# Kernel optimization log

Hardware: AMD Instinct MI355X
Metric: run time of the kernel (lower is better)

## Reference

```python
import jax, jax.numpy as jnp
import numpy as np

B, N, K, S_IN, S_OUT, C, FD = 32, 325, 20, 12, 12, 10, 64
ALPHA = 0.5  # LeakyReLU negative slope

def leaky(x):
    return jnp.where(x >= 0, x, ALPHA * x)

def setup_inputs() -> dict:
    key = jax.random.key(0)
    ks = jax.random.split(key, 9)
    s = 0.2
    return {
        "fushed_features": jax.random.normal(ks[0], (B, N, FD), jnp.float32),
        "input_data": jax.random.normal(ks[1], (B, N, S_IN), jnp.float32),
        "w_W": jax.random.normal(ks[2], (S_IN, S_OUT), jnp.float32) * s,
        "w_b": jax.random.normal(ks[3], (S_OUT,), jnp.float32) * s,
        "a1_W": jax.random.normal(ks[4], (2 * S_OUT, 4 * S_OUT), jnp.float32) * s,
        "a1_b": jax.random.normal(ks[5], (4 * S_OUT,), jnp.float32) * s,
        "a2_W": jax.random.normal(ks[6], (4 * S_OUT, C), jnp.float32) * s,
        "a2_b": jax.random.normal(ks[7], (C,), jnp.float32) * s,
        "adj_mx_topk_index": jax.random.randint(ks[8], (B, N, K), 0, N),
    }

def reference(fushed_features, input_data, w_W, w_b, a1_W, a1_b, a2_W, a2_b, adj_mx_topk_index):
    # w_net: Linear + LeakyReLU -> wh [B,N,S_OUT]
    wh = leaky(input_data @ w_W + w_b)
    # a_net on cat([wh_i, wh_j]): split first linear to avoid materializing [B,N,N,2*S_OUT]
    hx = wh @ a1_W[:S_OUT]   # contribution of wh_x (row node i)
    hy = wh @ a1_W[S_OUT:]   # contribution of wh_y (col node j)
    hidden = leaky(hx[:, :, None, :] + hy[:, None, :, :] + a1_b)   # [B,N,N,4*S_OUT]
    attention = leaky(hidden @ a2_W + a2_b)                        # [B,N,N,C]
    idx = adj_mx_topk_index                                        # [B,N,K]
    # gather top-k neighbors along dim 2
    idx_c = jnp.broadcast_to(idx[..., None], idx.shape + (attention.shape[-1],))
    attention_mask = jnp.take_along_axis(attention, idx_c, axis=2)  # [B,N,K,C]
    attention_mask = jax.nn.softmax(attention_mask, axis=-1)
    # gather neighbor features: wh_expand_top_k[b,i,k] = wh[b, idx[b,i,k]]
    wh_topk = wh[jnp.arange(wh.shape[0])[:, None, None], idx]       # [B,N,K,S_OUT]
    # output = attention_mask^T @ wh_topk
    output_data = jnp.einsum('bnkc,bnks->bncs', attention_mask, wh_topk)
    # clustering loss on detached neighbor features (cosine similarity)
    wt = jax.lax.stop_gradient(wh_topk)
    wtn = wt / (jnp.linalg.norm(wt, axis=-1, keepdims=True) + 1e-8)
    dist_mat = jnp.einsum('bnks,bnls->bnkl', wtn, wtn)              # [B,N,K,K]
    same = (dist_mat >= 0.5).astype(dist_mat.dtype)
    diff = 1.0 - same
    prob = jnp.einsum('bnkc,bnlc->bnkl', attention_mask, attention_mask)
    prob = jnp.clip(prob, 1e-4, 1.0 - 1e-4)
    logp = jnp.log(prob)
    cl = -(same * logp - diff * logp)
    cluster_loss = (cl.sum((-1, -2)) - jnp.trace(cl, axis1=-2, axis2=-1)).mean()
    return output_data, cluster_loss, dist_mat.mean(), wh.mean()
```

## Files before the change

### kernel.cpp

```cpp
#include <hip/hip_runtime.h>
#include <math.h>

#define Bdim 32
#define Ndim 325
#define Kdim 20
#define Sdim 12
#define Cdim 10
#define Hdim 48
#define NB   (Bdim*Ndim)
#define OUT_SCALARS (NB*Cdim*Sdim)
#define Tpairs (Kdim*(Kdim-1)/2)
#define BN_BLOCKS (NB/4)
#define NODE_BLOCKS 260
#define NPB 40

#define O_WH  0
#define O_HX  (O_WH + NB*Sdim)
#define O_HY  (O_HX + NB*Hdim)
#define O_PCL (O_HY + NB*Hdim)
#define O_PDS (O_PCL + BN_BLOCKS)
#define O_PWH (O_PDS + BN_BLOCKS)
#define WS_BASE_FLOATS (O_PWH + NODE_BLOCKS)

__device__ __forceinline__ float leaky(float x) { return x >= 0.f ? x : 0.5f * x; }

__global__ __launch_bounds__(512)
void node_kernel(const float* __restrict__ x,
                 const float* __restrict__ wW, const float* __restrict__ wb,
                 const float* __restrict__ A1, const float* __restrict__ b1,
                 float* __restrict__ ws)
{
    __shared__ float s_wh[NPB][Sdim];
    __shared__ float s_r[8];
    const int tid = threadIdx.x;
    const int base = blockIdx.x * NPB;

    float v = 0.f;
    if (tid < NPB * Sdim) {
        const int n = tid / Sdim, s = tid - n * Sdim;
        const float* xr = x + (size_t)(base + n) * Sdim;
        float acc = wb[s];
        #pragma unroll
        for (int i = 0; i < Sdim; i++) acc += xr[i] * wW[i * Sdim + s];
        acc = leaky(acc);
        s_wh[n][s] = acc;
        ws[O_WH + (size_t)(base + n) * Sdim + s] = acc;
        v += acc;
    }
    __syncthreads();

    #pragma unroll
    for (int rep = 0; rep < 8; rep++) {
        const int e = tid + rep * 512;
        if (e < NPB * 96) {
            const int n = e / 96, r = e - n * 96;
            const int which = r / Hdim, d = r - which * Hdim;
            const float4 w0 = *(const float4*)&s_wh[n][0];
            const float4 w1 = *(const float4*)&s_wh[n][4];
            const float4 w2 = *(const float4*)&s_wh[n][8];
            const float* Ac = A1 + (which * Sdim) * Hdim + d;
            float acc = which ? 0.f : b1[d];
            acc += w0.x*Ac[0*Hdim] + w0.y*Ac[1*Hdim] + w0.z*Ac[2*Hdim] + w0.w*Ac[3*Hdim]
                 + w1.x*Ac[4*Hdim] + w1.y*Ac[5*Hdim] + w1.z*Ac[6*Hdim] + w1.w*Ac[7*Hdim]
                 + w2.x*Ac[8*Hdim] + w2.y*Ac[9*Hdim] + w2.z*Ac[10*Hdim] + w2.w*Ac[11*Hdim];
            ws[(which ? O_HY : O_HX) + (size_t)(base + n) * Hdim + d] = acc;
        }
    }

    #pragma unroll
    for (int off = 32; off > 0; off >>= 1) v += __shfl_down(v, off);
    if ((tid & 63) == 0) s_r[tid >> 6] = v;
    __syncthreads();
    if (tid == 0) {
        float t = 0.f;
        #pragma unroll
        for (int i = 0; i < 8; i++) t += s_r[i];
        ws[O_PWH + blockIdx.x] = t;
    }
}

__global__ __launch_bounds__(256)
void mega_kernel(const int* __restrict__ topk,
                 const float* __restrict__ A2, const float* __restrict__ b2,
                 float* __restrict__ ws, float* __restrict__ out)
{
    __shared__ float s_A2  [Hdim * 12];
    __shared__ float s_whj [4][Kdim][12];
    __shared__ float s_am  [4][Kdim][12];
    __shared__ float s_invn[4][Kdim];
    __shared__ float s_red[2][4];

    const int tid = threadIdx.x;
    const int slot = tid >> 6, t = tid & 63;

    #pragma unroll
    for (int e = tid; e < Hdim * Cdim; e += 256) {
        const int d = e / Cdim, c = e - d * Cdim;
        s_A2[d * 12 + c] = A2[e];
    }
    __syncthreads();

    if (tid < 160) {
        const int e = tid >> 1, half = tid & 1;
        const int gid = blockIdx.x * 80 + e;
        const int bn_e = gid / Kdim;
        const int b_e  = bn_e / Ndim;
        const int j    = topk[gid];
        const int ek   = e / 20, kk = e - ek * 20;

        const float4* hx4 = (const float4*)(ws + O_HX + (size_t)bn_e * Hdim) + half * 6;
        const float4* hy4 = (const float4*)(ws + O_HY + ((size_t)b_e * Ndim + j) * Hdim) + half * 6;

        float acc[Cdim];
        #pragma unroll
        for (int c = 0; c < Cdim; c++) acc[c] = 0.f;
        #pragma unroll
        for (int q = 0; q < 6; q++) {
            const float4 xv = hx4[q], yv = hy4[q];
            const float hh[4] = { leaky(xv.x + yv.x), leaky(xv.y + yv.y),
                                  leaky(xv.z + yv.z), leaky(xv.w + yv.w) };
            #pragma unroll
            for (int i = 0; i < 4; i++) {
                const int d = half * 24 + q * 4 + i;
                const float* Ar = &s_A2[d * 12];
                const float4 r0 = *(const float4*)(Ar + 0);
                const float4 r1 = *(const float4*)(Ar + 4);
                const float2 r2 = *(const float2*)(Ar + 8);
                const float h = hh[i];
                acc[0] += h * r0.x; acc[1] += h * r0.y;
                acc[2] += h * r0.z; acc[3] += h * r0.w;
                acc[4] += h * r1.x; acc[5] += h * r1.y;
                acc[6] += h * r1.z; acc[7] += h * r1.w;
                acc[8] += h * r2.x; acc[9] += h * r2.y;
            }
        }
        float full[Cdim];
        #pragma unroll
        for (int c = 0; c < Cdim; c++) full[c] = acc[c] + __shfl_xor(acc[c], 1);
        if (half == 0) {
            float m = -1e30f;
            #pragma unroll
            for (int c = 0; c < Cdim; c++) { full[c] = leaky(full[c] + b2[c]); m = fmaxf(m, full[c]); }
            float sum = 0.f;
            #pragma unroll
            for (int c = 0; c < Cdim; c++) { full[c] = __expf(full[c] - m); sum += full[c]; }
            const float inv = 1.f / sum;
            *(float4*)&s_am[ek][kk][0] = make_float4(full[0]*inv, full[1]*inv, full[2]*inv, full[3]*inv);
            *(float4*)&s_am[ek][kk][4] = make_float4(full[4]*inv, full[5]*inv, full[6]*inv, full[7]*inv);
            *(float4*)&s_am[ek][kk][8] = make_float4(full[8]*inv, full[9]*inv, 0.f, 0.f);
        }
    } else {
        for (int i = tid - 160; i < 240; i += 96) {
            const int kf = i / 3, q = i - kf * 3;
            const int sl = kf / 20, k = kf - sl * 20;
            const int gidx = blockIdx.x * 80 + kf;
            const int bn_i = gidx / Kdim;
            const int b_i  = bn_i / Ndim;
            const int j    = topk[gidx];
            const float4 v = *(const float4*)(ws + O_WH + ((size_t)b_i * Ndim + j) * Sdim + q * 4);
            *(float4*)&s_whj[sl][k][q * 4] = v;
        }
    }
    __syncthreads();

    const int bn = blockIdx.x * 4 + slot;
    float cl = 0.f, ds = 0.f;

    if (t < Kdim) {
        const float4 w0 = *(const float4*)&s_whj[slot][t][0];
        const float4 w1 = *(const float4*)&s_whj[slot][t][4];
        const float4 w2 = *(const float4*)&s_whj[slot][t][8];
        const float nn = w0.x*w0.x + w0.y*w0.y + w0.z*w0.z + w0.w*w0.w
                       + w1.x*w1.x + w1.y*w1.y + w1.z*w1.z + w1.w*w1.w
                       + w2.x*w2.x + w2.y*w2.y + w2.z*w2.z + w2.w*w2.w;
        const float invn = 1.f / (sqrtf(nn) + 1e-8f);
        s_invn[slot][t] = invn;
        ds += nn * invn * invn;
    } else if (t < Kdim + 30) {
        const int e = t - Kdim, c = e / 3, sq = e - c * 3;
        float4 o = make_float4(0.f, 0.f, 0.f, 0.f);
        #pragma unroll
        for (int k = 0; k < Kdim; k++) {
            const float a = s_am[slot][k][c];
            const float4 w = *(const float4*)&s_whj[slot][k][sq * 4];
            o.x += a * w.x; o.y += a * w.y; o.z += a * w.z; o.w += a * w.w;
        }
        *(float4*)(out + (size_t)bn * (Cdim * Sdim) + c * Sdim + sq * 4) = o;
    }
    __builtin_amdgcn_wave_barrier();

    #pragma unroll
    for (int it = 0; it < 3; it++) {
        const int e = t + it * 64;
        if (e < Tpairs) {
            const int r = Tpairs - 1 - e;
            const int m = (int)((sqrtf((float)(8 * r + 1)) - 1.f) * 0.5f + 1e-4f);
            const int k = Kdim - 2 - m;
            const int l = Kdim - 1 - (r - (m * (m + 1)) / 2);

            const float4 a0 = *(const float4*)&s_whj[slot][k][0];
            const float4 a1 = *(const float4*)&s_whj[slot][k][4];
            const float4 a2 = *(const float4*)&s_whj[slot][k][8];
            const float4 c0 = *(const float4*)&s_whj[slot][l][0];
            const float4 c1 = *(const float4*)&s_whj[slot][l][4];
            const float4 c2 = *(const float4*)&s_whj[slot][l][8];
            const float draw = a0.x*c0.x + a0.y*c0.y + a0.z*c0.z + a0.w*c0.w
                             + a1.x*c1.x + a1.y*c1.y + a1.z*c1.z + a1.w*c1.w
                             + a2.x*c2.x + a2.y*c2.y + a2.z*c2.z + a2.w*c2.w;
            const float d = draw * s_invn[slot][k] * s_invn[slot][l];

            const float4 p0 = *(const float4*)&s_am[slot][k][0];
            const float4 p1 = *(const float4*)&s_am[slot][k][4];
            const float4 p2 = *(const float4*)&s_am[slot][k][8];
            const float4 q0 = *(const float4*)&s_am[slot][l][0];
            const float4 q1 = *(const float4*)&s_am[slot][l][4];
            const float4 q2 = *(const float4*)&s_am[slot][l][8];
            float p = p0.x*q0.x + p0.y*q0.y + p0.z*q0.z + p0.w*q0.w
                    + p1.x*q1.x + p1.y*q1.y + p1.z*q1.z + p1.w*q1.w
                    + p2.x*q2.x + p2.y*q2.y + p2.z*q2.z + p2.w*q2.w;

            p = fminf(fmaxf(p, 1e-4f), 1.f - 1e-4f);
            const float lp = __logf(p);
            ds += 2.f * d;
            cl += 2.f * ((d >= 0.5f) ? -lp : lp);
        }
    }

    #pragma unroll
    for (int off = 32; off > 0; off >>= 1) {
        cl += __shfl_down(cl, off);
        ds += __shfl_down(ds, off);
    }
    if (t == 0) { s_red[0][slot] = cl; s_red[1][slot] = ds; }
    __syncthreads();
    if (tid == 0) {
        ws[O_PCL + blockIdx.x] = s_red[0][0] + s_red[0][1] + s_red[0][2] + s_red[0][3];
        ws[O_PDS + blockIdx.x] = s_red[1][0] + s_red[1][1] + s_red[1][2] + s_red[1][3];
    }
}

__global__ __launch_bounds__(1024)
void finalize(const float* __restrict__ ws, float* __restrict__ out)
{
    const int t = threadIdx.x;
    float cl = 0.f, ds = 0.f, wm = 0.f;
    for (int i = t; i < BN_BLOCKS; i += 1024) {
        cl += ws[O_PCL + i]; ds += ws[O_PDS + i];
    }
    if (t < NODE_BLOCKS) wm = ws[O_PWH + t];
    #pragma unroll
    for (int off = 32; off > 0; off >>= 1) {
        cl += __shfl_down(cl, off);
        ds += __shfl_down(ds, off);
        wm += __shfl_down(wm, off);
    }
    __shared__ float r[3][16];
    const int w = t >> 6, lane = t & 63;
    if (lane == 0) { r[0][w] = cl; r[1][w] = ds; r[2][w] = wm; }
    __syncthreads();
    if (t == 0) {
        float c = 0.f, d = 0.f, m = 0.f;
        #pragma unroll
        for (int i = 0; i < 16; i++) { c += r[0][i]; d += r[1][i]; m += r[2][i]; }
        out[OUT_SCALARS + 0] = c * (1.f / (float)NB);
        out[OUT_SCALARS + 1] = d * (1.f / ((float)NB * Kdim * Kdim));
        out[OUT_SCALARS + 2] = m * (1.f / ((float)NB * Sdim));
    }
}

__global__ void zero_scalars(float* out) {
    const int t = threadIdx.x;
    if (t < 3) out[OUT_SCALARS + t] = 0.f;
}

__global__ __launch_bounds__(64)
void fused_kernel(const float* __restrict__ input_data,
                  const float* __restrict__ w_W,  const float* __restrict__ w_b,
                  const float* __restrict__ a1_W, const float* __restrict__ a1_b,
                  const float* __restrict__ a2_W, const float* __restrict__ a2_b,
                  const int*   __restrict__ topk,
                  float* __restrict__ out)
{
    __shared__ float s_wW[Sdim * Sdim];
    __shared__ float s_wb[Sdim];
    __shared__ float s_A1[2 * Sdim * Hdim];
    __shared__ float s_b1[Hdim];
    __shared__ float s_A2f[Hdim * Cdim];
    __shared__ float s_b2f[Cdim];
    __shared__ float s_whs[Sdim];
    __shared__ float s_hx[Hdim];
    __shared__ float s_whj[Kdim][Sdim + 1];
    __shared__ float s_hid[Kdim][Hdim + 1];
    __shared__ float s_am [Kdim][Cdim + 1];
    __shared__ float s_wtn[Kdim][Sdim + 1];
    __shared__ int   s_idx[Kdim];

    const int t = threadIdx.x, bn = blockIdx.x, b = bn / Ndim;

    for (int i = t; i < Sdim * Sdim; i += 64)      s_wW[i] = w_W[i];
    if (t < Sdim)                                  s_wb[t] = w_b[t];
    for (int i = t; i < 2 * Sdim * Hdim; i += 64)  s_A1[i] = a1_W[i];
    if (t < Hdim)                                  s_b1[t] = a1_b[t];
    for (int i = t; i < Hdim * Cdim; i += 64)      s_A2f[i] = a2_W[i];
    if (t < Cdim)                                  s_b2f[t] = a2_b[t];
    if (t < Kdim)                                  s_idx[t] = topk[(size_t)bn * Kdim + t];
    __syncthreads();

    const float* xs = input_data + (size_t)bn * Sdim;
    if (t < Sdim) {
        float acc = s_wb[t];
        #pragma unroll
        for (int i = 0; i < Sdim; i++) acc += xs[i] * s_wW[i * Sdim + t];
        s_whs[t] = leaky(acc);
    }
    __syncthreads();

    if (t < Hdim) {
        float acc = 0.f;
        #pragma unroll
        for (int s = 0; s < Sdim; s++) acc += s_whs[s] * s_A1[s * Hdim + t];
        s_hx[t] = acc;
    }
    for (int e = t; e < Kdim * Sdim; e += 64) {
        const int k = e / Sdim, ss = e - k * Sdim;
        const float* xj = input_data + ((size_t)b * Ndim + s_idx[k]) * Sdim;
        float acc = s_wb[ss];
        #pragma unroll
        for (int i = 0; i < Sdim; i++) acc += xj[i] * s_wW[i * Sdim + ss];
        s_whj[k][ss] = leaky(acc);
    }
    __syncthreads();

    for (int e = t; e < Kdim * Hdim; e += 64) {
        const int k = e / Hdim, d = e - k * Hdim;
        float acc = s_hx[d] + s_b1[d];
        #pragma unroll
        for (int s = 0; s < Sdim; s++) acc += s_whj[k][s] * s_A1[(Sdim + s) * Hdim + d];
        s_hid[k][d] = leaky(acc);
    }
    __syncthreads();

    for (int e = t; e < Kdim * Cdim; e += 64) {
        const int k = e / Cdim, c = e - k * Cdim;
        float acc = s_b2f[c];
        #pragma unroll
        for (int d = 0; d < Hdim; d++) acc += s_hid[k][d] * s_A2f[d * Cdim + c];
        s_am[k][c] = leaky(acc);
    }
    __syncthreads();

    if (t < Kdim) {
        float m = -1e30f;
        #pragma unroll
        for (int c = 0; c < Cdim; c++) m = fmaxf(m, s_am[t][c]);
        float ex[Cdim]; float sum = 0.f;
        #pragma unroll
        for (int c = 0; c < Cdim; c++) { ex[c] = expf(s_am[t][c] - m); sum += ex[c]; }
        const float inv = 1.f / sum;
        #pragma unroll
        for (int c = 0; c < Cdim; c++) s_am[t][c] = ex[c] * inv;
        float nn = 0.f;
        #pragma unroll
        for (int s = 0; s < Sdim; s++) nn += s_whj[t][s] * s_whj[t][s];
        const float invn = 1.f / (sqrtf(nn) + 1e-8f);
        #pragma unroll
        for (int s = 0; s < Sdim; s++) s_wtn[t][s] = s_whj[t][s] * invn;
    }
    __syncthreads();

    float* op = out + (size_t)bn * (Cdim * Sdim);
    for (int e = t; e < Cdim * Sdim; e += 64) {
        const int c = e / Sdim, ss = e - c * Sdim;
        float acc = 0.f;
        #pragma unroll
        for (int k = 0; k < Kdim; k++) acc += s_am[k][c] * s_whj[k][ss];
        op[e] = acc;
    }

    float cl = 0.f, ds = 0.f;
    for (int e = t; e < Kdim * Kdim; e += 64) {
        const int k = e / Kdim, l = e - k * Kdim;
        float d = 0.f;
        #pragma unroll
        for (int s = 0; s < Sdim; s++) d += s_wtn[k][s] * s_wtn[l][s];
        ds += d;
        if (k != l) {
            float p = 0.f;
            #pragma unroll
            for (int c = 0; c < Cdim; c++) p += s_am[k][c] * s_am[l][c];
            p = fminf(fmaxf(p, 1e-4f), 1.f - 1e-4f);
            const float lp = logf(p);
            cl += (d >= 0.5f) ? -lp : lp;
        }
    }
    float whl = (t < Sdim) ? s_whs[t] : 0.f;
    #pragma unroll
    for (int off = 32; off > 0; off >>= 1) {
        cl  += __shfl_down(cl,  off);
        ds  += __shfl_down(ds,  off);
        whl += __shfl_down(whl, off);
    }
    if (t == 0) {
        atomicAdd(&out[OUT_SCALARS + 0], cl  * (1.f / (float)NB));
        atomicAdd(&out[OUT_SCALARS + 1], ds  * (1.f / ((float)NB * Kdim * Kdim)));
        atomicAdd(&out[OUT_SCALARS + 2], whl * (1.f / ((float)NB * Sdim)));
    }
}

extern "C" void kernel_launch(void* const* d_in, const int* in_sizes, int n_in,
                              void* d_out, int out_size, void* d_ws, size_t ws_size,
                              hipStream_t stream) {
    (void)in_sizes; (void)n_in; (void)out_size;
    const float* input_data = (const float*)d_in[1];
    const float* w_W  = (const float*)d_in[2];
    const float* w_b  = (const float*)d_in[3];
    const float* a1_W = (const float*)d_in[4];
    const float* a1_b = (const float*)d_in[5];
    const float* a2_W = (const float*)d_in[6];
    const float* a2_b = (const float*)d_in[7];
    const int*   topk = (const int*)d_in[8];
    float* out = (float*)d_out;
    float* ws  = (float*)d_ws;

    if (ws_size >= (size_t)WS_BASE_FLOATS * sizeof(float)) {
        hipLaunchKernelGGL(node_kernel, dim3(NODE_BLOCKS), dim3(512), 0, stream,
                           input_data, w_W, w_b, a1_W, a1_b, ws);
        hipLaunchKernelGGL(mega_kernel, dim3(BN_BLOCKS), dim3(256), 0, stream,
                           topk, a2_W, a2_b, ws, out);
        hipLaunchKernelGGL(finalize, dim3(1), dim3(1024), 0, stream, ws, out);
    } else {
        hipLaunchKernelGGL(zero_scalars, dim3(1), dim3(64), 0, stream, out);
        hipLaunchKernelGGL(fused_kernel, dim3(NB), dim3(64), 0, stream,
                           input_data, w_W, w_b, a1_W, a1_b, a2_W, a2_b, topk, out);
    }
}
```

Measured before the change: 104.6 us.

## Drop finalize kernel via atomics, tile pair loss 2x2, stage topk in LDS

Removes the separate finalize launch. Node_kernel now zeroes the scalar outputs, and mega_kernel adds its per-block partial sums straight into them with atomics; block 0 also reduces the wh mean. The pairwise cluster-loss loop is replaced by 220 threads that each handle a 2x2 tile of (k,l) pairs, reusing operand loads across the tile, and a full block barrier replaces the wave barrier. Top-k indices are staged once in shared memory, and node_kernel moves to 256-thread blocks. In exchange there are about 2.6k float atomics on three addresses, and the summation order becomes nondeterministic.

```diff
diff --git a/kernel.cpp b/kernel.cpp
--- a/kernel.cpp
+++ b/kernel.cpp
@@ -9,7 +9,6 @@
 #define Hdim 48
 #define NB   (Bdim*Ndim)
 #define OUT_SCALARS (NB*Cdim*Sdim)
-#define Tpairs (Kdim*(Kdim-1)/2)
 #define BN_BLOCKS (NB/4)
 #define NODE_BLOCKS 260
 #define NPB 40
@@ -24,59 +23,66 @@
 
 __device__ __forceinline__ float leaky(float x) { return x >= 0.f ? x : 0.5f * x; }
 
-__global__ __launch_bounds__(512)
+__global__ __launch_bounds__(256)
 void node_kernel(const float* __restrict__ x,
                  const float* __restrict__ wW, const float* __restrict__ wb,
                  const float* __restrict__ A1, const float* __restrict__ b1,
-                 float* __restrict__ ws)
+                 float* __restrict__ ws, float* __restrict__ out)
 {
     __shared__ float s_wh[NPB][Sdim];
-    __shared__ float s_r[8];
+    __shared__ float s_r[4];
     const int tid = threadIdx.x;
     const int base = blockIdx.x * NPB;
 
+    if (blockIdx.x == 0 && tid < 3) out[OUT_SCALARS + tid] = 0.f;
+
     float v = 0.f;
-    if (tid < NPB * Sdim) {
-        const int n = tid / Sdim, s = tid - n * Sdim;
-        const float* xr = x + (size_t)(base + n) * Sdim;
-        float acc = wb[s];
-        #pragma unroll
-        for (int i = 0; i < Sdim; i++) acc += xr[i] * wW[i * Sdim + s];
-        acc = leaky(acc);
-        s_wh[n][s] = acc;
-        ws[O_WH + (size_t)(base + n) * Sdim + s] = acc;
-        v += acc;
-    }
-    __syncthreads();
-
     #pragma unroll
-    for (int rep = 0; rep < 8; rep++) {
-        const int e = tid + rep * 512;
-        if (e < NPB * 96) {
-            const int n = e / 96, r = e - n * 96;
-            const int which = r / Hdim, d = r - which * Hdim;
-            const float4 w0 = *(const float4*)&s_wh[n][0];
-            const float4 w1 = *(const float4*)&s_wh[n][4];
-            const float4 w2 = *(const float4*)&s_wh[n][8];
-            const float* Ac = A1 + (which * Sdim) * Hdim + d;
-            float acc = which ? 0.f : b1[d];
-            acc += w0.x*Ac[0*Hdim] + w0.y*Ac[1*Hdim] + w0.z*Ac[2*Hdim] + w0.w*Ac[3*Hdim]
-                 + w1.x*Ac[4*Hdim] + w1.y*Ac[5*Hdim] + w1.z*Ac[6*Hdim] + w1.w*Ac[7*Hdim]
-                 + w2.x*Ac[8*Hdim] + w2.y*Ac[9*Hdim] + w2.z*Ac[10*Hdim] + w2.w*Ac[11*Hdim];
-            ws[(which ? O_HY : O_HX) + (size_t)(base + n) * Hdim + d] = acc;
-        }
+    for (int rep = 0; rep < 2; rep++) {
+        const int e = tid + rep * 256;
+        if (e < NPB * Sdim) {
+            const int n = e / Sdim, s = e - n * Sdim;
+            const float* xr = x + (size_t)(base + n) * Sdim;
+            float acc = wb[s];
+            #pragma unroll
+            for (int i = 0; i < Sdim; i++) acc += xr[i] * wW[i * Sdim + s];
+            acc = leaky(acc);
+            s_wh[n][s] = acc;
+            ws[O_WH + (size_t)(base + n) * Sdim + s] = acc;
+            v += acc;
+        }
+    }
+    __syncthreads();
+
+    #pragma unroll
+    for (int rep = 0; rep < 15; rep++) {
+        const int e = tid + rep * 256;
+        const int n = e / 96, r = e - n * 96;
+        const int which = r / Hdim, d = r - which * Hdim;
+        const float4 w0 = *(const float4*)&s_wh[n][0];
+        const float4 w1 = *(const float4*)&s_wh[n][4];
+        const float4 w2 = *(const float4*)&s_wh[n][8];
+        const float* Ac = A1 + (which * Sdim) * Hdim + d;
+        float acc = which ? 0.f : b1[d];
+        acc += w0.x*Ac[0*Hdim] + w0.y*Ac[1*Hdim] + w0.z*Ac[2*Hdim] + w0.w*Ac[3*Hdim]
+             + w1.x*Ac[4*Hdim] + w1.y*Ac[5*Hdim] + w1.z*Ac[6*Hdim] + w1.w*Ac[7*Hdim]
+             + w2.x*Ac[8*Hdim] + w2.y*Ac[9*Hdim] + w2.z*Ac[10*Hdim] + w2.w*Ac[11*Hdim];
+        ws[(which ? O_HY : O_HX) + (size_t)(base + n) * Hdim + d] = acc;
     }
 
     #pragma unroll
     for (int off = 32; off > 0; off >>= 1) v += __shfl_down(v, off);
     if ((tid & 63) == 0) s_r[tid >> 6] = v;
     __syncthreads();
-    if (tid == 0) {
-        float t = 0.f;
-        #pragma unroll
-        for (int i = 0; i < 8; i++) t += s_r[i];
-        ws[O_PWH + blockIdx.x] = t;
-    }
+    if (tid == 0) ws[O_PWH + blockIdx.x] = s_r[0] + s_r[1] + s_r[2] + s_r[3];
+}
+
+__device__ __forceinline__ float dot12(const float4& a0, const float4& a1, const float4& a2,
+                                       const float4& b0, const float4& b1, const float4& b2)
+{
+    return a0.x*b0.x + a0.y*b0.y + a0.z*b0.z + a0.w*b0.w
+         + a1.x*b1.x + a1.y*b1.y + a1.z*b1.z + a1.w*b1.w
+         + a2.x*b2.x + a2.y*b2.y + a2.z*b2.z + a2.w*b2.w;
 }
 
 __global__ __launch_bounds__(256)
@@ -85,6 +91,7 @@
                  float* __restrict__ ws, float* __restrict__ out)
 {
     __shared__ float s_A2  [Hdim * 12];
+    __shared__ int   s_topk[80];
     __shared__ float s_whj [4][Kdim][12];
     __shared__ float s_am  [4][Kdim][12];
     __shared__ float s_invn[4][Kdim];
@@ -93,10 +100,16 @@
     const int tid = threadIdx.x;
     const int slot = tid >> 6, t = tid & 63;
 
-    #pragma unroll
-    for (int e = tid; e < Hdim * Cdim; e += 256) {
-        const int d = e / Cdim, c = e - d * Cdim;
-        s_A2[d * 12 + c] = A2[e];
+    if (tid < 120) {
+        const int e0 = tid * 4;
+        #pragma unroll
+        for (int u = 0; u < 4; u++) {
+            const int e = e0 + u;
+            const int d = e / Cdim, c = e - d * Cdim;
+            s_A2[d * 12 + c] = A2[e];
+        }
+    } else if (tid < 200) {
+        s_topk[tid - 120] = topk[blockIdx.x * 80 + (tid - 120)];
     }
     __syncthreads();
 
@@ -105,7 +118,7 @@
         const int gid = blockIdx.x * 80 + e;
         const int bn_e = gid / Kdim;
         const int b_e  = bn_e / Ndim;
-        const int j    = topk[gid];
+        const int j    = s_topk[e];
         const int ek   = e / 20, kk = e - ek * 20;
 
         const float4* hx4 = (const float4*)(ws + O_HX + (size_t)bn_e * Hdim) + half * 6;
@@ -153,10 +166,9 @@
         for (int i = tid - 160; i < 240; i += 96) {
             const int kf = i / 3, q = i - kf * 3;
             const int sl = kf / 20, k = kf - sl * 20;
-            const int gidx = blockIdx.x * 80 + kf;
-            const int bn_i = gidx / Kdim;
+            const int bn_i = (blockIdx.x * 80 + kf) / Kdim;
             const int b_i  = bn_i / Ndim;
-            const int j    = topk[gidx];
+            const int j    = s_topk[kf];
             const float4 v = *(const float4*)(ws + O_WH + ((size_t)b_i * Ndim + j) * Sdim + q * 4);
             *(float4*)&s_whj[sl][k][q * 4] = v;
         }
@@ -170,9 +182,7 @@
         const float4 w0 = *(const float4*)&s_whj[slot][t][0];
         const float4 w1 = *(const float4*)&s_whj[slot][t][4];
         const float4 w2 = *(const float4*)&s_whj[slot][t][8];
-        const float nn = w0.x*w0.x + w0.y*w0.y + w0.z*w0.z + w0.w*w0.w
-                       + w1.x*w1.x + w1.y*w1.y + w1.z*w1.z + w1.w*w1.w
-                       + w2.x*w2.x + w2.y*w2.y + w2.z*w2.z + w2.w*w2.w;
+        const float nn = dot12(w0, w1, w2, w0, w1, w2);
         const float invn = 1.f / (sqrtf(nn) + 1e-8f);
         s_invn[slot][t] = invn;
         ds += nn * invn * invn;
@@ -187,42 +197,50 @@
         }
         *(float4*)(out + (size_t)bn * (Cdim * Sdim) + c * Sdim + sq * 4) = o;
     }
-    __builtin_amdgcn_wave_barrier();
-
-    #pragma unroll
-    for (int it = 0; it < 3; it++) {
-        const int e = t + it * 64;
-        if (e < Tpairs) {
-            const int r = Tpairs - 1 - e;
-            const int m = (int)((sqrtf((float)(8 * r + 1)) - 1.f) * 0.5f + 1e-4f);
-            const int k = Kdim - 2 - m;
-            const int l = Kdim - 1 - (r - (m * (m + 1)) / 2);
-
-            const float4 a0 = *(const float4*)&s_whj[slot][k][0];
-            const float4 a1 = *(const float4*)&s_whj[slot][k][4];
-            const float4 a2 = *(const float4*)&s_whj[slot][k][8];
-            const float4 c0 = *(const float4*)&s_whj[slot][l][0];
-            const float4 c1 = *(const float4*)&s_whj[slot][l][4];
-            const float4 c2 = *(const float4*)&s_whj[slot][l][8];
-            const float draw = a0.x*c0.x + a0.y*c0.y + a0.z*c0.z + a0.w*c0.w
-                             + a1.x*c1.x + a1.y*c1.y + a1.z*c1.z + a1.w*c1.w
-                             + a2.x*c2.x + a2.y*c2.y + a2.z*c2.z + a2.w*c2.w;
-            const float d = draw * s_invn[slot][k] * s_invn[slot][l];
-
-            const float4 p0 = *(const float4*)&s_am[slot][k][0];
-            const float4 p1 = *(const float4*)&s_am[slot][k][4];
-            const float4 p2 = *(const float4*)&s_am[slot][k][8];
-            const float4 q0 = *(const float4*)&s_am[slot][l][0];
-            const float4 q1 = *(const float4*)&s_am[slot][l][4];
-            const float4 q2 = *(const float4*)&s_am[slot][l][8];
-            float p = p0.x*q0.x + p0.y*q0.y + p0.z*q0.z + p0.w*q0.w
-                    + p1.x*q1.x + p1.y*q1.y + p1.z*q1.z + p1.w*q1.w
-                    + p2.x*q2.x + p2.y*q2.y + p2.z*q2.z + p2.w*q2.w;
-
-            p = fminf(fmaxf(p, 1e-4f), 1.f - 1e-4f);
-            const float lp = __logf(p);
-            ds += 2.f * d;
-            cl += 2.f * ((d >= 0.5f) ? -lp : lp);
+    __syncthreads();
+
+    if (tid < 220) {
+        const int slot_l = tid / 55;
+        const int t55 = tid - slot_l * 55;
+        const int gi = (int)((21.0f - sqrtf((float)(441 - 8 * t55))) * 0.5f);
+        const int gj = gi + (t55 - (gi * (21 - gi)) / 2);
+        const int i0 = 2 * gi, j0 = 2 * gj;
+        const bool diag = (gi == gj);
+
+        const float4* W = (const float4*)&s_whj[slot_l][0][0];
+        const float4* P = (const float4*)&s_am [slot_l][0][0];
+
+        float4 wi[2][3], wj[2][3], pi[2][3], pj[2][3];
+        #pragma unroll
+        for (int u = 0; u < 2; u++) {
+            #pragma unroll
+            for (int q = 0; q < 3; q++) {
+                wi[u][q] = W[(i0 + u) * 3 + q];
+                wj[u][q] = W[(j0 + u) * 3 + q];
+                pi[u][q] = P[(i0 + u) * 3 + q];
+                pj[u][q] = P[(j0 + u) * 3 + q];
+            }
+        }
+        const float inv_i0 = s_invn[slot_l][i0], inv_i1 = s_invn[slot_l][i0 + 1];
+        const float inv_j0 = s_invn[slot_l][j0], inv_j1 = s_invn[slot_l][j0 + 1];
+        const float inv_i[2] = { inv_i0, inv_i1 };
+        const float inv_j[2] = { inv_j0, inv_j1 };
+
+        #pragma unroll
+        for (int ii = 0; ii < 2; ii++) {
+            #pragma unroll
+            for (int jj = 0; jj < 2; jj++) {
+                const float wgt = diag ? ((ii == 0 && jj == 1) ? 2.f : 0.f) : 2.f;
+                const float draw = dot12(wi[ii][0], wi[ii][1], wi[ii][2],
+                                         wj[jj][0], wj[jj][1], wj[jj][2]);
+                const float d = draw * inv_i[ii] * inv_j[jj];
+                float p = dot12(pi[ii][0], pi[ii][1], pi[ii][2],
+                                pj[jj][0], pj[jj][1], pj[jj][2]);
+                p = fminf(fmaxf(p, 1e-4f), 1.f - 1e-4f);
+                const float lp = __logf(p);
+                ds += wgt * d;
+                cl += wgt * ((d >= 0.5f) ? -lp : lp);
+            }
         }
     }
 
@@ -234,37 +252,18 @@
     if (t == 0) { s_red[0][slot] = cl; s_red[1][slot] = ds; }
     __syncthreads();
     if (tid == 0) {
-        ws[O_PCL + blockIdx.x] = s_red[0][0] + s_red[0][1] + s_red[0][2] + s_red[0][3];
-        ws[O_PDS + blockIdx.x] = s_red[1][0] + s_red[1][1] + s_red[1][2] + s_red[1][3];
-    }
-}
-
-__global__ __launch_bounds__(1024)
-void finalize(const float* __restrict__ ws, float* __restrict__ out)
-{
-    const int t = threadIdx.x;
-    float cl = 0.f, ds = 0.f, wm = 0.f;
-    for (int i = t; i < BN_BLOCKS; i += 1024) {
-        cl += ws[O_PCL + i]; ds += ws[O_PDS + i];
-    }
-    if (t < NODE_BLOCKS) wm = ws[O_PWH + t];
-    #pragma unroll
-    for (int off = 32; off > 0; off >>= 1) {
-        cl += __shfl_down(cl, off);
-        ds += __shfl_down(ds, off);
-        wm += __shfl_down(wm, off);
-    }
-    __shared__ float r[3][16];
-    const int w = t >> 6, lane = t & 63;
-    if (lane == 0) { r[0][w] = cl; r[1][w] = ds; r[2][w] = wm; }
-    __syncthreads();
-    if (t == 0) {
-        float c = 0.f, d = 0.f, m = 0.f;
-        #pragma unroll
-        for (int i = 0; i < 16; i++) { c += r[0][i]; d += r[1][i]; m += r[2][i]; }
-        out[OUT_SCALARS + 0] = c * (1.f / (float)NB);
-        out[OUT_SCALARS + 1] = d * (1.f / ((float)NB * Kdim * Kdim));
-        out[OUT_SCALARS + 2] = m * (1.f / ((float)NB * Sdim));
+        const float c = s_red[0][0] + s_red[0][1] + s_red[0][2] + s_red[0][3];
+        const float d = s_red[1][0] + s_red[1][1] + s_red[1][2] + s_red[1][3];
+        atomicAdd(&out[OUT_SCALARS + 0], c * (1.f / (float)NB));
+        atomicAdd(&out[OUT_SCALARS + 1], d * (1.f / ((float)NB * Kdim * Kdim)));
+    }
+
+    if (blockIdx.x == 0 && tid < 64) {
+        float wm = 0.f;
+        for (int i = tid; i < NODE_BLOCKS; i += 64) wm += ws[O_PWH + i];
+        #pragma unroll
+        for (int off = 32; off > 0; off >>= 1) wm += __shfl_down(wm, off);
+        if (tid == 0) atomicAdd(&out[OUT_SCALARS + 2], wm * (1.f / ((float)NB * Sdim)));
     }
 }
 
@@ -423,11 +422,10 @@
     float* ws  = (float*)d_ws;
 
     if (ws_size >= (size_t)WS_BASE_FLOATS * sizeof(float)) {
-        hipLaunchKernelGGL(node_kernel, dim3(NODE_BLOCKS), dim3(512), 0, stream,
-                           input_data, w_W, w_b, a1_W, a1_b, ws);
+        hipLaunchKernelGGL(node_kernel, dim3(NODE_BLOCKS), dim3(256), 0, stream,
+                           input_data, w_W, w_b, a1_W, a1_b, ws, out);
         hipLaunchKernelGGL(mega_kernel, dim3(BN_BLOCKS), dim3(256), 0, stream,
                            topk, a2_W, a2_b, ws, out);
-        hipLaunchKernelGGL(finalize, dim3(1), dim3(1024), 0, stream, ws, out);
     } else {
         hipLaunchKernelGGL(zero_scalars, dim3(1), dim3(64), 0, stream, out);
         hipLaunchKernelGGL(fused_kernel, dim3(NB), dim3(64), 0, stream,
```

Result: slower. 158.7 us (+51.6%).
